# Optimization experiments

Measured on AMD Instinct MI355X. Metric: run time of the kernel, lower is better.

Reference implementation:

```python
import jax, jax.numpy as jnp
import numpy as np

B, N, S, K = 32, 2048, 64, 128   # clouds, pts/cloud, fps centers (ratio=64/2048), max neighbors
R = 0.2                          # radius ball-query
SLOPE = 0.2                      # LeakyReLU negative slope
C_CONV = [3, 64, 128, 512]       # PointConv local nn
D_FEAT = 512


def leaky(x):
    return jnp.where(x >= 0, x, SLOPE * x)


def _init_linear(key, din, dout):
    kw, kb = jax.random.split(key)
    lim = 1.0 / np.sqrt(din)
    W = jax.random.uniform(kw, (din, dout), minval=-lim, maxval=lim, dtype=jnp.float32)
    b = jax.random.uniform(kb, (dout,), minval=-lim, maxval=lim, dtype=jnp.float32)
    return W, b


def setup_inputs() -> dict:
    key = jax.random.key(0)
    ks = jax.random.split(key, 6)
    pos = jax.random.uniform(ks[0], (B * N, 3), dtype=jnp.float32)
    batch = (jnp.arange(B * N, dtype=jnp.int32) // N)
    W1, b1 = _init_linear(ks[1], 3, 64)
    W2, b2 = _init_linear(ks[2], 64, 128)
    W3, b3 = _init_linear(ks[3], 128, 512)
    W4, b4 = _init_linear(ks[4], D_FEAT + 3, 512)
    W5, b5 = _init_linear(ks[5], 512, 1024)
    return {"pos": pos, "batch": batch,
            "W1": W1, "b1": b1, "W2": W2, "b2": b2, "W3": W3, "b3": b3,
            "W4": W4, "b4": b4, "W5": W5, "b5": b5}


def _fps_one(p):
    """Deterministic farthest point sampling on one cloud p:[N,3] -> idx:[S]."""
    d0 = jnp.sum((p - p[0]) ** 2, axis=-1)

    def step(dists, _):
        nxt = jnp.argmax(dists).astype(jnp.int32)
        dists = jnp.minimum(dists, jnp.sum((p - p[nxt]) ** 2, axis=-1))
        return dists, nxt

    _, rest = jax.lax.scan(step, d0, None, length=S - 1)
    return jnp.concatenate([jnp.zeros((1,), jnp.int32), rest])


def _encoder(pos, W1, b1, W2, b2, W3, b3, W4, b4, W5, b5):
    pts = pos.reshape(B, N, 3)
    idx = jax.vmap(_fps_one)(pts)                                   # [B,S] local fps indices
    centers = jnp.take_along_axis(pts, idx[:, :, None], axis=1)     # [B,S,3]

    # radius ball query (first-by-index up to K neighbors, like torch_cluster cap)
    d2 = jnp.sum((centers[:, :, None, :] - pts[:, None, :, :]) ** 2, axis=-1)  # [B,S,N]
    inball = d2 < R * R
    keys = jnp.where(inball, jnp.arange(N, dtype=jnp.int32)[None, None, :], N)
    nbr = jnp.sort(keys, axis=-1)[:, :, :K]                          # [B,S,K]
    valid = nbr < N
    nbr = jnp.where(valid, nbr, 0)

    # PointConv: gather relative positions -> MLP -> masked max aggregation
    nbr_pos = jnp.take_along_axis(pts[:, None, :, :], nbr[..., None], axis=2)  # [B,S,K,3]
    rel = nbr_pos - centers[:, :, None, :]
    h = leaky(rel @ W1 + b1)
    h = leaky(h @ W2 + b2)
    h = leaky(h @ W3 + b3)                                           # [B,S,K,512]
    h = jnp.where(valid[..., None], h, -jnp.inf)
    feat = jnp.max(h, axis=2)                                        # [B,S,512] (self always in ball)

    g = jnp.concatenate([feat, centers], axis=-1).reshape(B * S, D_FEAT + 3)
    g = leaky(g @ W4 + b4)
    out = g @ W5 + b5                                                # [B*S,1024]
    mean, logvar = out[:, :512], out[:, 512:]
    std = jnp.exp(0.5 * logvar)

    # global edge indices (x_idx = neighbor point id, y_idx = center id), -1 padded
    x_idx = jnp.where(valid, nbr + jnp.arange(B, dtype=jnp.int32)[:, None, None] * N, -1).reshape(-1)
    y_idx = jnp.where(valid, jnp.arange(B * S, dtype=jnp.int32).reshape(B, S, 1), -1).reshape(-1)
    return mean, std, x_idx, y_idx


def reference(pos, batch, W1, b1, W2, b2, W3, b3, W4, b4, W5, b5):
    # batch is implied by the fixed [B,N] layout (sorted, equal-size clouds)
    return _encoder(pos, W1, b1, W2, b2, W3, b3, W4, b4, W5, b5)
```

## Files before the change

### kernel.cpp

```cpp
#include <hip/hip_runtime.h>
#include <hip/hip_bf16.h>

#define NB 32
#define NP 2048
#define NS 64
#define NK 128

#define MEAN_OFF 0
#define STD_OFF  1048576
#define XIDX_OFF 2097152
#define YIDX_OFF 2359296

#define GA_LD 576

typedef __attribute__((ext_vector_type(4)))  short s4;
typedef __attribute__((ext_vector_type(8)))  short short8;
typedef __attribute__((ext_vector_type(16))) float f32x16;

static __device__ __forceinline__ float leaky(float x){ return x >= 0.0f ? x : 0.2f * x; }

static __device__ __forceinline__ unsigned short bf16u(float v){
    __hip_bfloat16 h = __float2bfloat16(v);
    return *(unsigned short*)&h;
}

static __device__ __forceinline__ float d2s(float ax,float ay,float az,float bx,float by,float bz){
    float dx = __fsub_rn(ax,bx), dy = __fsub_rn(ay,by), dz = __fsub_rn(az,bz);
    return __fadd_rn(__fadd_rn(__fmul_rn(dx,dx),__fmul_rn(dy,dy)),__fmul_rn(dz,dz));
}

__global__ __launch_bounds__(256) void fps_prep_kernel(const float* __restrict__ pos,
                                                       float* __restrict__ centersWs,
                                                       const float* __restrict__ W2,
                                                       const float* __restrict__ W3,
                                                       const float* __restrict__ W4,
                                                       const float* __restrict__ W5,
                                                       __hip_bfloat16* __restrict__ W2T,
                                                       __hip_bfloat16* __restrict__ W3T,
                                                       __hip_bfloat16* __restrict__ W4T,
                                                       __hip_bfloat16* __restrict__ W5T)
{
    if (blockIdx.x >= NB) {
        int g = (blockIdx.x - NB)*256 + threadIdx.x;
        if (g < 65536) {
            int c = g >> 7, i = g & 127;
            int byte = c*256 + ((i*2) ^ ((c&15)<<4));
            W3T[byte>>1] = __float2bfloat16(W3[(size_t)i*512 + c]);
        }
        if (g < 8192) {
            int i = g >> 6, j = g & 63;
            W2T[g] = __float2bfloat16(W2[(size_t)j*128 + i]);
        }
        for (int e = g; e < 512*GA_LD; e += 131072) {
            int n = e / GA_LD, k = e - n*GA_LD;
            float v = (k < 515) ? W4[(size_t)k*512 + n] : 0.0f;
            W4T[e] = __float2bfloat16(v);
        }
        for (int e = g; e < 1024*512; e += 131072) {
            int n = e >> 9, k = e & 511;
            W5T[e] = __float2bfloat16(W5[(size_t)k*1024 + n]);
        }
        return;
    }

    int b = blockIdx.x;
    int t = threadIdx.x;
    __shared__ float px[NP], py[NP], pz[NP];
    __shared__ float redv[4];
    __shared__ int   redi[4];
    __shared__ int   jsh;

    const float* pb = pos + (size_t)b * NP * 3;
    for (int n = t; n < NP; n += 256) {
        px[n] = pb[n*3+0]; py[n] = pb[n*3+1]; pz[n] = pb[n*3+2];
    }
    __syncthreads();

    float p0x = px[0], p0y = py[0], p0z = pz[0];
    float dl[8];
    #pragma unroll
    for (int q = 0; q < 8; q++) {
        int n = t + q*256;
        dl[q] = d2s(px[n],py[n],pz[n], p0x,p0y,p0z);
    }
    if (t == 0) {
        centersWs[(b*NS)*3+0] = p0x;
        centersWs[(b*NS)*3+1] = p0y;
        centersWs[(b*NS)*3+2] = p0z;
    }

    for (int s = 1; s < NS; s++) {
        float bv = -1.0f; int bi = 0;
        #pragma unroll
        for (int q = 0; q < 8; q++) {
            int n = t + q*256;
            if (dl[q] > bv) { bv = dl[q]; bi = n; }
        }
        #pragma unroll
        for (int m = 32; m > 0; m >>= 1) {
            float ov = __shfl_xor(bv, m);
            int   oi = __shfl_xor(bi, m);
            if (ov > bv || (ov == bv && oi < bi)) { bv = ov; bi = oi; }
        }
        int w = t >> 6;
        if ((t & 63) == 0) { redv[w] = bv; redi[w] = bi; }
        __syncthreads();
        if (t == 0) {
            float v = redv[0]; int i = redi[0];
            #pragma unroll
            for (int k = 1; k < 4; k++) {
                if (redv[k] > v || (redv[k] == v && redi[k] < i)) { v = redv[k]; i = redi[k]; }
            }
            jsh = i;
            centersWs[(b*NS+s)*3+0] = px[i];
            centersWs[(b*NS+s)*3+1] = py[i];
            centersWs[(b*NS+s)*3+2] = pz[i];
        }
        __syncthreads();
        int j = jsh;
        float cx = px[j], cy = py[j], cz = pz[j];
        #pragma unroll
        for (int q = 0; q < 8; q++) {
            int n = t + q*256;
            dl[q] = fminf(dl[q], d2s(px[n],py[n],pz[n], cx,cy,cz));
        }
    }
}

__global__ __launch_bounds__(256, 3) void ball_mlp_kernel(
    const float* __restrict__ pos,
    const float* __restrict__ W1, const float* __restrict__ b1,
    const float* __restrict__ b2, const float* __restrict__ b3,
    const __hip_bfloat16* __restrict__ W2Tp,
    const __hip_bfloat16* __restrict__ W3Tp,
    const float* __restrict__ centersWs,
    float* __restrict__ out,
    __hip_bfloat16* __restrict__ gAb)
{
    __shared__ char smem[52752];
    char*  h1s  = smem;
    char*  h2s  = smem + 16384;
    float* relL = (float*)(smem + 49152);
    int*   nbL  = (int*)(smem + 49152);
    float* b2s  = (float*)(smem + 51200);
    int*   nb   = (int*)(smem + 51712);
    float* red  = (float*)(smem + 52224);
    int*   cntW4= (int*)(smem + 52736);

    const short* W2T  = (const short*)W2Tp;
    const char*  W3Tb = (const char*)W3Tp;

    int r = blockIdx.x, b = r >> 6, tid = threadIdx.x;
    int l = tid & 63, w = tid >> 6;
    int l31 = l & 31;
    int hsel = l >> 5;
    int jsel8 = hsel * 8;
    int colsel = hsel * 16;

    float cx = centersWs[r*3+0], cy = centersWs[r*3+1], cz = centersWs[r*3+2];

    int wi = w & 1, wk = w >> 1;
    short8 aW[2][4];
    #pragma unroll
    for (int rt = 0; rt < 2; rt++) {
        int ia = (2*wi + rt)*32 + l31;
        #pragma unroll
        for (int ks = 0; ks < 4; ks++)
            aW[rt][ks] = *(const short8*)(W2T + ia*64 + ks*16 + jsel8);
    }

    const float* pb = pos + (size_t)b * NP * 3;
    {
        int myCnt = 0;
        #pragma unroll
        for (int c = 0; c < 8; c++) {
            int n = w*512 + c*64 + l;
            float x = pb[n*3+0], y = pb[n*3+1], z = pb[n*3+2];
            bool in = d2s(cx,cy,cz, x,y,z) < 0.04f;
            unsigned long long m = __ballot(in);
            int before = __popcll(m & ((1ull << l) - 1ull));
            int p = myCnt + before;
            if (in && p < NK) nbL[w*NK + p] = n;
            myCnt += (int)__popcll(m);
        }
        if (l == 0) cntW4[w] = myCnt;
    }
    __syncthreads();

    int c0 = cntW4[0], c1 = cntW4[1], c2 = cntW4[2], c3 = cntW4[3];
    int cnt = c0 + c1 + c2 + c3;
    cnt = cnt > NK ? NK : cnt;

    int nv = 0;
    if (tid < NK) {
        bool valid = tid < cnt;
        int seg = 0, off = 0;
        if (tid >= c0)           { seg = 1; off = c0; }
        if (tid >= c0 + c1)      { seg = 2; off = c0 + c1; }
        if (tid >= c0 + c1 + c2) { seg = 3; off = c0 + c1 + c2; }
        if (valid) nv = nbL[seg*NK + (tid - off)];
        out[XIDX_OFF + r*NK + tid] = valid ? (float)(nv + b*NP) : -1.0f;
        out[YIDX_OFF + r*NK + tid] = valid ? (float)r : -1.0f;
    }
    __syncthreads();

    if (tid < NK) {
        const float* pp = pb + (size_t)nv*3;
        relL[tid*4+0] = pp[0] - cx;
        relL[tid*4+1] = pp[1] - cy;
        relL[tid*4+2] = pp[2] - cz;
        relL[tid*4+3] = 0.0f;
        b2s[tid] = b2[tid];
    }
    __syncthreads();

    {
        int jg = (tid & 15) * 4;
        float4 w0 = *(const float4*)&W1[jg];
        float4 w1 = *(const float4*)&W1[64 + jg];
        float4 w2 = *(const float4*)&W1[128 + jg];
        float4 bb = *(const float4*)&b1[jg];
        #pragma unroll
        for (int e = 0; e < 8; e++) {
            int k = (tid >> 4) + e*16;
            float4 r4 = *(const float4*)&relL[k*4];
            s4 pk;
            pk[0] = (short)bf16u(leaky(bb.x + r4.x*w0.x + r4.y*w1.x + r4.z*w2.x));
            pk[1] = (short)bf16u(leaky(bb.y + r4.x*w0.y + r4.y*w1.y + r4.z*w2.y));
            pk[2] = (short)bf16u(leaky(bb.z + r4.x*w0.z + r4.y*w1.z + r4.z*w2.z));
            pk[3] = (short)bf16u(leaky(bb.w + r4.x*w0.w + r4.y*w1.w + r4.z*w2.w));
            *(s4*)(h1s + k*128 + ((jg*2) ^ ((k&7)<<4))) = pk;
        }
    }
    __syncthreads();

    {
        f32x16 acc[2][2];
        #pragma unroll
        for (int q = 0; q < 16; q++) { acc[0][0][q]=0.f; acc[0][1][q]=0.f; acc[1][0][q]=0.f; acc[1][1][q]=0.f; }
        int kc0 = (2*wk)*32 + l31, kc1 = kc0 + 32;
        #pragma unroll
        for (int ks = 0; ks < 4; ks++) {
            int bc = ks*32 + colsel;
            short8 bh0 = *(short8*)(h1s + kc0*128 + (bc ^ ((kc0&7)<<4)));
            short8 bh1 = *(short8*)(h1s + kc1*128 + (bc ^ ((kc1&7)<<4)));
            acc[0][0] = __builtin_amdgcn_mfma_f32_32x32x16_bf16(aW[0][ks], bh0, acc[0][0], 0, 0, 0);
            acc[0][1] = __builtin_amdgcn_mfma_f32_32x32x16_bf16(aW[0][ks], bh1, acc[0][1], 0, 0, 0);
            acc[1][0] = __builtin_amdgcn_mfma_f32_32x32x16_bf16(aW[1][ks], bh0, acc[1][0], 0, 0, 0);
            acc[1][1] = __builtin_amdgcn_mfma_f32_32x32x16_bf16(aW[1][ks], bh1, acc[1][1], 0, 0, 0);
        }
        #pragma unroll
        for (int rt = 0; rt < 2; rt++) {
            int ibase = (2*wi + rt)*32 + 4*hsel;
            float4 bias[4];
            #pragma unroll
            for (int g = 0; g < 4; g++) bias[g] = *(const float4*)&b2s[ibase + g*8];
            #pragma unroll
            for (int ct = 0; ct < 2; ct++) {
                int k = (ct == 0) ? kc0 : kc1;
                #pragma unroll
                for (int g = 0; g < 4; g++) {
                    s4 pk;
                    pk[0] = (short)bf16u(leaky(acc[rt][ct][g*4+0] + bias[g].x));
                    pk[1] = (short)bf16u(leaky(acc[rt][ct][g*4+1] + bias[g].y));
                    pk[2] = (short)bf16u(leaky(acc[rt][ct][g*4+2] + bias[g].z));
                    pk[3] = (short)bf16u(leaky(acc[rt][ct][g*4+3] + bias[g].w));
                    *(s4*)(h2s + k*256 + (((ibase + g*8)*2) ^ ((k&15)<<4))) = pk;
                }
            }
        }
    }
    __syncthreads();

    {
        const char* s0 = W3Tb + 0*8192 + w*2048 + l*16;
        char* d0 = h1s + 0 + w*2048;
        __builtin_amdgcn_global_load_lds((const __attribute__((address_space(1))) void*)(s0),
                                         (__attribute__((address_space(3))) void*)(d0), 16, 0, 0);
        __builtin_amdgcn_global_load_lds((const __attribute__((address_space(1))) void*)(s0 + 1024),
                                         (__attribute__((address_space(3))) void*)(d0 + 1024), 16, 0, 0);
        const char* s1 = W3Tb + 1*8192 + w*2048 + l*16;
        char* d1 = h1s + 8192 + w*2048;
        __builtin_amdgcn_global_load_lds((const __attribute__((address_space(1))) void*)(s1),
                                         (__attribute__((address_space(3))) void*)(d1), 16, 0, 0);
        __builtin_amdgcn_global_load_lds((const __attribute__((address_space(1))) void*)(s1 + 1024),
                                         (__attribute__((address_space(3))) void*)(d1 + 1024), 16, 0, 0);
    }

    short8 a3[8];
    {
        int row = w*32 + l31;
        #pragma unroll
        for (int ks = 0; ks < 8; ks++) {
            int bc = ks*32 + colsel;
            a3[ks] = *(short8*)(h2s + row*256 + (bc ^ ((row&15)<<4)));
        }
    }

    int kb0 = w*32 + 4*hsel;
    #pragma unroll
    for (int t = 0; t < 16; t++) {
        if (t < 15) { asm volatile("s_waitcnt vmcnt(2)" ::: "memory"); }
        else        { asm volatile("s_waitcnt vmcnt(0)" ::: "memory"); }
        __builtin_amdgcn_sched_barrier(0);
        __builtin_amdgcn_s_barrier();
        __builtin_amdgcn_sched_barrier(0);

        char* buf = h1s + (t & 1)*8192;
        f32x16 acc;
        #pragma unroll
        for (int q = 0; q < 16; q++) acc[q] = 0.f;
        #pragma unroll
        for (int ks = 0; ks < 8; ks++) {
            int bc = ks*32 + colsel;
            short8 bv = *(short8*)(buf + l31*256 + (bc ^ ((l31&15)<<4)));
            acc = __builtin_amdgcn_mfma_f32_32x32x16_bf16(a3[ks], bv, acc, 0, 0, 0);
        }
        float m = -INFINITY;
        #pragma unroll
        for (int reg = 0; reg < 16; reg++) {
            int kloc = (reg&3) + 8*(reg>>2);
            if (kb0 + kloc < cnt) m = fmaxf(m, acc[reg]);
        }
        m = fmaxf(m, __shfl_xor(m, 32));
        if (l < 32) red[w*32 + l31] = m;

        __builtin_amdgcn_s_barrier();
        __builtin_amdgcn_sched_barrier(0);
        if (tid < 32) {
            float m4 = fmaxf(fmaxf(red[tid], red[32 + tid]), fmaxf(red[64 + tid], red[96 + tid]));
            float bc3 = b3[t*32 + tid];
            gAb[(size_t)r*GA_LD + t*32 + tid] = __float2bfloat16(leaky(m4 + bc3));
        }
        __builtin_amdgcn_sched_barrier(0);
        if (t + 2 < 16) {
            const char* src = W3Tb + (t+2)*8192 + w*2048 + l*16;
            char* dst = buf + w*2048;
            __builtin_amdgcn_global_load_lds((const __attribute__((address_space(1))) void*)(src),
                                             (__attribute__((address_space(3))) void*)(dst), 16, 0, 0);
            __builtin_amdgcn_global_load_lds((const __attribute__((address_space(1))) void*)(src + 1024),
                                             (__attribute__((address_space(3))) void*)(dst + 1024), 16, 0, 0);
        }
    }

    if (tid < 64) {
        float v = 0.0f;
        if (tid == 0) v = cx; else if (tid == 1) v = cy; else if (tid == 2) v = cz;
        gAb[(size_t)r*GA_LD + 512 + tid] = __float2bfloat16(v);
    }
}

__global__ __launch_bounds__(256) void fc1_kernel(const __hip_bfloat16* __restrict__ gAb,
                                                  const __hip_bfloat16* __restrict__ W4T,
                                                  const float* __restrict__ b4,
                                                  __hip_bfloat16* __restrict__ g2b)
{
    __shared__ char smem[16384];
    char* As = smem;
    char* Bs = smem + 8192;

    int bx = blockIdx.x & 7;
    int by = blockIdx.x >> 3;
    int tid = threadIdx.x;
    int l = tid & 63, w = tid >> 6;
    int wm = w & 1, wn = w >> 1;
    int colsel = (l >> 5) * 16;

    f32x16 acc;
    #pragma unroll
    for (int q = 0; q < 16; q++) acc[q] = 0.f;

    int ra = wm*32 + (l & 31);
    int rn = wn*32 + (l & 31);

    for (int kb = 0; kb < GA_LD; kb += 64) {
        #pragma unroll
        for (int it = 0; it < 2; it++) {
            int e = it*256 + tid;
            int row = e >> 3, seg = e & 7;
            short8 va = *(const short8*)(gAb + (size_t)(by*64 + row)*GA_LD + kb + seg*8);
            *(short8*)(As + row*128 + ((seg*16) ^ ((row&7)<<4))) = va;
            short8 vb = *(const short8*)(W4T + (size_t)(bx*64 + row)*GA_LD + kb + seg*8);
            *(short8*)(Bs + row*128 + ((seg*16) ^ ((row&7)<<4))) = vb;
        }
        __syncthreads();
        #pragma unroll
        for (int ks = 0; ks < 4; ks++) {
            int bc = ks*32 + colsel;
            short8 av = *(short8*)(As + ra*128 + (bc ^ ((ra&7)<<4)));
            short8 bv = *(short8*)(Bs + rn*128 + (bc ^ ((rn&7)<<4)));
            acc = __builtin_amdgcn_mfma_f32_32x32x16_bf16(av, bv, acc, 0, 0, 0);
        }
        __syncthreads();
    }

    int col = bx*64 + wn*32 + (l & 31);
    float bcol = b4[col];
    int rbase = by*64 + wm*32 + 4*(l>>5);
    #pragma unroll
    for (int reg = 0; reg < 16; reg++) {
        int row = rbase + (reg&3) + 8*(reg>>2);
        g2b[(size_t)row*512 + col] = __float2bfloat16(leaky(acc[reg] + bcol));
    }
}

__global__ __launch_bounds__(256) void fc2_kernel(const __hip_bfloat16* __restrict__ g2b,
                                                  const __hip_bfloat16* __restrict__ W5T,
                                                  const float* __restrict__ b5,
                                                  float* __restrict__ out)
{
    __shared__ char smem[16384];
    char* As = smem;
    char* Bs = smem + 8192;

    int bx = blockIdx.x & 15;
    int by = blockIdx.x >> 4;
    int tid = threadIdx.x;
    int l = tid & 63, w = tid >> 6;
    int wm = w & 1, wn = w >> 1;
    int colsel = (l >> 5) * 16;

    f32x16 acc;
    #pragma unroll
    for (int q = 0; q < 16; q++) acc[q] = 0.f;

    int ra = wm*32 + (l & 31);
    int rn = wn*32 + (l & 31);

    for (int kb = 0; kb < 512; kb += 64) {
        #pragma unroll
        for (int it = 0; it < 2; it++) {
            int e = it*256 + tid;
            int row = e >> 3, seg = e & 7;
            short8 va = *(const short8*)(g2b + (size_t)(by*64 + row)*512 + kb + seg*8);
            *(short8*)(As + row*128 + ((seg*16) ^ ((row&7)<<4))) = va;
            short8 vb = *(const short8*)(W5T + (size_t)(bx*64 + row)*512 + kb + seg*8);
            *(short8*)(Bs + row*128 + ((seg*16) ^ ((row&7)<<4))) = vb;
        }
        __syncthreads();
        #pragma unroll
        for (int ks = 0; ks < 4; ks++) {
            int bc = ks*32 + colsel;
            short8 av = *(short8*)(As + ra*128 + (bc ^ ((ra&7)<<4)));
            short8 bv = *(short8*)(Bs + rn*128 + (bc ^ ((rn&7)<<4)));
            acc = __builtin_amdgcn_mfma_f32_32x32x16_bf16(av, bv, acc, 0, 0, 0);
        }
        __syncthreads();
    }

    int col = bx*64 + wn*32 + (l & 31);
    float bcol = b5[col];
    int rbase = by*64 + wm*32 + 4*(l>>5);
    #pragma unroll
    for (int reg = 0; reg < 16; reg++) {
        int row = rbase + (reg&3) + 8*(reg>>2);
        float v = acc[reg] + bcol;
        if (col < 512) {
            out[MEAN_OFF + (size_t)row*512 + col] = v;
        } else {
            out[STD_OFF + (size_t)row*512 + (col - 512)] = expf(0.5f*v);
        }
    }
}

extern "C" void kernel_launch(void* const* d_in, const int* in_sizes, int n_in,
                              void* d_out, int out_size, void* d_ws, size_t ws_size,
                              hipStream_t stream) {
    const float* pos = (const float*)d_in[0];
    const float* W1  = (const float*)d_in[2];
    const float* b1  = (const float*)d_in[3];
    const float* W2  = (const float*)d_in[4];
    const float* b2  = (const float*)d_in[5];
    const float* W3  = (const float*)d_in[6];
    const float* b3  = (const float*)d_in[7];
    const float* W4  = (const float*)d_in[8];
    const float* b4  = (const float*)d_in[9];
    const float* W5  = (const float*)d_in[10];
    const float* b5  = (const float*)d_in[11];
    float* out = (float*)d_out;

    char* ws = (char*)d_ws;
    float* centersWs = (float*)(ws);
    __hip_bfloat16* gAb = (__hip_bfloat16*)(ws + 1081344);
    __hip_bfloat16* g2b = (__hip_bfloat16*)(ws + 3440640);
    __hip_bfloat16* W2T = (__hip_bfloat16*)(ws + 5537792);
    __hip_bfloat16* W3T = (__hip_bfloat16*)(ws + 5554176);
    __hip_bfloat16* W4T = (__hip_bfloat16*)(ws + 5685248);
    __hip_bfloat16* W5T = (__hip_bfloat16*)(ws + 6275072);

    hipLaunchKernelGGL(fps_prep_kernel, dim3(NB + 512), dim3(256), 0, stream,
                       pos, centersWs, W2, W3, W4, W5, W2T, W3T, W4T, W5T);
    hipLaunchKernelGGL(ball_mlp_kernel, dim3(NB*NS), dim3(256), 0, stream,
                       pos, W1,b1, b2,b3, W2T, W3T, centersWs, out, gAb);
    hipLaunchKernelGGL(fc1_kernel, dim3(256), dim3(256), 0, stream, gAb, W4T, b4, g2b);
    hipLaunchKernelGGL(fc2_kernel, dim3(512), dim3(256), 0, stream, g2b, W5T, b5, out);
}
```

Before: 159.6 us.

## Deepen W3 prefetch to four buffers and defer per-chunk max reduction

The layer-3 loop now streams W3 chunks through four LDS buffers with a prefetch distance of three instead of two. It also drops the per-iteration barrier and reduction: each wave writes its partial maxima into a larger LDS area, and one reduction after the loop produces all 512 features, with b3 cached in LDS. Separately, the FPS kernel moves to 512-thread blocks with 4 points per thread and a reduction over 8 waves. This trades extra LDS use and a changed grid shape for fewer barriers and more load latency hiding.

Result: slower. 175.8 us (+10.1%).

```diff
diff --git a/kernel.cpp b/kernel.cpp
--- a/kernel.cpp
+++ b/kernel.cpp
@@ -29,7 +29,7 @@
     return __fadd_rn(__fadd_rn(__fmul_rn(dx,dx),__fmul_rn(dy,dy)),__fmul_rn(dz,dz));
 }
 
-__global__ __launch_bounds__(256) void fps_prep_kernel(const float* __restrict__ pos,
+__global__ __launch_bounds__(512) void fps_prep_kernel(const float* __restrict__ pos,
                                                        float* __restrict__ centersWs,
                                                        const float* __restrict__ W2,
                                                        const float* __restrict__ W3,
@@ -41,7 +41,7 @@
                                                        __hip_bfloat16* __restrict__ W5T)
 {
     if (blockIdx.x >= NB) {
-        int g = (blockIdx.x - NB)*256 + threadIdx.x;
+        int g = (blockIdx.x - NB)*512 + threadIdx.x;
         if (g < 65536) {
             int c = g >> 7, i = g & 127;
             int byte = c*256 + ((i*2) ^ ((c&15)<<4));
@@ -66,21 +66,21 @@
     int b = blockIdx.x;
     int t = threadIdx.x;
     __shared__ float px[NP], py[NP], pz[NP];
-    __shared__ float redv[4];
-    __shared__ int   redi[4];
+    __shared__ float redv[8];
+    __shared__ int   redi[8];
     __shared__ int   jsh;
 
     const float* pb = pos + (size_t)b * NP * 3;
-    for (int n = t; n < NP; n += 256) {
+    for (int n = t; n < NP; n += 512) {
         px[n] = pb[n*3+0]; py[n] = pb[n*3+1]; pz[n] = pb[n*3+2];
     }
     __syncthreads();
 
     float p0x = px[0], p0y = py[0], p0z = pz[0];
-    float dl[8];
-    #pragma unroll
-    for (int q = 0; q < 8; q++) {
-        int n = t + q*256;
+    float dl[4];
+    #pragma unroll
+    for (int q = 0; q < 4; q++) {
+        int n = t + q*512;
         dl[q] = d2s(px[n],py[n],pz[n], p0x,p0y,p0z);
     }
     if (t == 0) {
@@ -92,8 +92,8 @@
     for (int s = 1; s < NS; s++) {
         float bv = -1.0f; int bi = 0;
         #pragma unroll
-        for (int q = 0; q < 8; q++) {
-            int n = t + q*256;
+        for (int q = 0; q < 4; q++) {
+            int n = t + q*512;
             if (dl[q] > bv) { bv = dl[q]; bi = n; }
         }
         #pragma unroll
@@ -108,7 +108,7 @@
         if (t == 0) {
             float v = redv[0]; int i = redi[0];
             #pragma unroll
-            for (int k = 1; k < 4; k++) {
+            for (int k = 1; k < 8; k++) {
                 if (redv[k] > v || (redv[k] == v && redi[k] < i)) { v = redv[k]; i = redi[k]; }
             }
             jsh = i;
@@ -120,8 +120,8 @@
         int j = jsh;
         float cx = px[j], cy = py[j], cz = pz[j];
         #pragma unroll
-        for (int q = 0; q < 8; q++) {
-            int n = t + q*256;
+        for (int q = 0; q < 4; q++) {
+            int n = t + q*512;
             dl[q] = fminf(dl[q], d2s(px[n],py[n],pz[n], cx,cy,cz));
         }
     }
@@ -137,15 +137,15 @@
     float* __restrict__ out,
     __hip_bfloat16* __restrict__ gAb)
 {
-    __shared__ char smem[52752];
+    __shared__ char smem[53776];
     char*  h1s  = smem;
     char*  h2s  = smem + 16384;
     float* relL = (float*)(smem + 49152);
     int*   nbL  = (int*)(smem + 49152);
     float* b2s  = (float*)(smem + 51200);
-    int*   nb   = (int*)(smem + 51712);
-    float* red  = (float*)(smem + 52224);
-    int*   cntW4= (int*)(smem + 52736);
+    int*   cntW4= (int*)(smem + 51712);
+    float* b3s  = (float*)(smem + 51728);
+    float* red  = (float*)(smem + 32768);
 
     const short* W2T  = (const short*)W2Tp;
     const char*  W3Tb = (const char*)W3Tp;
@@ -185,6 +185,8 @@
         }
         if (l == 0) cntW4[w] = myCnt;
     }
+    b3s[tid] = b3[tid];
+    b3s[tid + 256] = b3[tid + 256];
     __syncthreads();
 
     int c0 = cntW4[0], c1 = cntW4[1], c2 = cntW4[2], c3 = cntW4[3];
@@ -272,20 +274,23 @@
     }
     __syncthreads();
 
-    {
-        const char* s0 = W3Tb + 0*8192 + w*2048 + l*16;
-        char* d0 = h1s + 0 + w*2048;
-        __builtin_amdgcn_global_load_lds((const __attribute__((address_space(1))) void*)(s0),
-                                         (__attribute__((address_space(3))) void*)(d0), 16, 0, 0);
-        __builtin_amdgcn_global_load_lds((const __attribute__((address_space(1))) void*)(s0 + 1024),
-                                         (__attribute__((address_space(3))) void*)(d0 + 1024), 16, 0, 0);
-        const char* s1 = W3Tb + 1*8192 + w*2048 + l*16;
-        char* d1 = h1s + 8192 + w*2048;
-        __builtin_amdgcn_global_load_lds((const __attribute__((address_space(1))) void*)(s1),
-                                         (__attribute__((address_space(3))) void*)(d1), 16, 0, 0);
-        __builtin_amdgcn_global_load_lds((const __attribute__((address_space(1))) void*)(s1 + 1024),
-                                         (__attribute__((address_space(3))) void*)(d1 + 1024), 16, 0, 0);
-    }
+    char* buf0 = h1s;
+    char* buf1 = h1s + 8192;
+    char* buf2 = smem + 16384;
+    char* buf3 = smem + 24576;
+
+#define STAGE_W3(CH, DST)                                                                              \
+    {                                                                                                  \
+        const char* _s = W3Tb + (CH)*8192 + w*2048 + l*16;                                             \
+        char* _d = (DST) + w*2048;                                                                     \
+        __builtin_amdgcn_global_load_lds((const __attribute__((address_space(1))) void*)(_s),          \
+                                         (__attribute__((address_space(3))) void*)(_d), 16, 0, 0);     \
+        __builtin_amdgcn_global_load_lds((const __attribute__((address_space(1))) void*)(_s + 1024),   \
+                                         (__attribute__((address_space(3))) void*)(_d + 1024), 16, 0, 0); \
+    }
+
+    STAGE_W3(0, buf0);
+    STAGE_W3(1, buf1);
 
     short8 a3[8];
     {
@@ -296,17 +301,26 @@
             a3[ks] = *(short8*)(h2s + row*256 + (bc ^ ((row&15)<<4)));
         }
     }
+    __syncthreads();
+    STAGE_W3(2, buf2);
 
     int kb0 = w*32 + 4*hsel;
     #pragma unroll
     for (int t = 0; t < 16; t++) {
-        if (t < 15) { asm volatile("s_waitcnt vmcnt(2)" ::: "memory"); }
-        else        { asm volatile("s_waitcnt vmcnt(0)" ::: "memory"); }
+        if (t <= 13)      { asm volatile("s_waitcnt vmcnt(4)" ::: "memory"); }
+        else if (t == 14) { asm volatile("s_waitcnt vmcnt(2)" ::: "memory"); }
+        else              { asm volatile("s_waitcnt vmcnt(0)" ::: "memory"); }
         __builtin_amdgcn_sched_barrier(0);
         __builtin_amdgcn_s_barrier();
         __builtin_amdgcn_sched_barrier(0);
 
-        char* buf = h1s + (t & 1)*8192;
+        if (t + 3 < 16) {
+            char* nbuf = ((t+3)&3) == 0 ? buf0 : ((t+3)&3) == 1 ? buf1 : ((t+3)&3) == 2 ? buf2 : buf3;
+            STAGE_W3(t+3, nbuf);
+        }
+        __builtin_amdgcn_sched_barrier(0);
+
+        char* buf = (t&3) == 0 ? buf0 : (t&3) == 1 ? buf1 : (t&3) == 2 ? buf2 : buf3;
         f32x16 acc;
         #pragma unroll
         for (int q = 0; q < 16; q++) acc[q] = 0.f;
@@ -323,31 +337,23 @@
             if (kb0 + kloc < cnt) m = fmaxf(m, acc[reg]);
         }
         m = fmaxf(m, __shfl_xor(m, 32));
-        if (l < 32) red[w*32 + l31] = m;
-
-        __builtin_amdgcn_s_barrier();
+        if (l < 32) red[w*512 + t*32 + l31] = m;
         __builtin_amdgcn_sched_barrier(0);
-        if (tid < 32) {
-            float m4 = fmaxf(fmaxf(red[tid], red[32 + tid]), fmaxf(red[64 + tid], red[96 + tid]));
-            float bc3 = b3[t*32 + tid];
-            gAb[(size_t)r*GA_LD + t*32 + tid] = __float2bfloat16(leaky(m4 + bc3));
-        }
-        __builtin_amdgcn_sched_barrier(0);
-        if (t + 2 < 16) {
-            const char* src = W3Tb + (t+2)*8192 + w*2048 + l*16;
-            char* dst = buf + w*2048;
-            __builtin_amdgcn_global_load_lds((const __attribute__((address_space(1))) void*)(src),
-                                             (__attribute__((address_space(3))) void*)(dst), 16, 0, 0);
-            __builtin_amdgcn_global_load_lds((const __attribute__((address_space(1))) void*)(src + 1024),
-                                             (__attribute__((address_space(3))) void*)(dst + 1024), 16, 0, 0);
-        }
-    }
-
+    }
+    __syncthreads();
+
+    #pragma unroll
+    for (int e = 0; e < 2; e++) {
+        int c = tid + e*256;
+        float m = fmaxf(fmaxf(red[c], red[512 + c]), fmaxf(red[1024 + c], red[1536 + c]));
+        gAb[(size_t)r*GA_LD + c] = __float2bfloat16(leaky(m + b3s[c]));
+    }
     if (tid < 64) {
         float v = 0.0f;
         if (tid == 0) v = cx; else if (tid == 1) v = cy; else if (tid == 2) v = cz;
         gAb[(size_t)r*GA_LD + 512 + tid] = __float2bfloat16(v);
     }
+#undef STAGE_W3
 }
 
 __global__ __launch_bounds__(256) void fc1_kernel(const __hip_bfloat16* __restrict__ gAb,
@@ -488,7 +494,7 @@
     __hip_bfloat16* W4T = (__hip_bfloat16*)(ws + 5685248);
     __hip_bfloat16* W5T = (__hip_bfloat16*)(ws + 6275072);
 
-    hipLaunchKernelGGL(fps_prep_kernel, dim3(NB + 512), dim3(256), 0, stream,
+    hipLaunchKernelGGL(fps_prep_kernel, dim3(NB + 256), dim3(512), 0, stream,
                        pos, centersWs, W2, W3, W4, W5, W2T, W3T, W4T, W5T);
     hipLaunchKernelGGL(ball_mlp_kernel, dim3(NB*NS), dim3(256), 0, stream,
                        pos, W1,b1, b2,b3, W2T, W3T, centersWs, out, gAb);
```
